# Kernel optimization log

Hardware: AMD Instinct MI355X
Metric: run time of the kernel (lower is better)

Reference implementation:

```python
import jax, jax.numpy as jnp
from jax import lax
import numpy as np

MB, N, QST, EPS = 512, 25, 11, 1e-5

def _coords():
    i = np.arange(25)
    # faithful to python3 true division: (i/5 - 2)/2.0, (i%5 - 2)/2.0
    c = np.stack([(i / 5 - 2) / 2.0, (i % 5 - 2) / 2.0], axis=-1).astype(np.float32)
    return jnp.asarray(c)  # [25, 2]

def _conv_bn(x, w, b, g, beta):
    # Conv2d(k=3, stride=2, pad=1) -> ReLU -> BatchNorm (training-mode batch stats)
    y = lax.conv_general_dilated(x, w, (2, 2), [(1, 1), (1, 1)],
                                 dimension_numbers=('NCHW', 'OIHW', 'NCHW'))
    y = jax.nn.relu(y + b[None, :, None, None])
    mean = y.mean(axis=(0, 2, 3), keepdims=True)
    var = y.var(axis=(0, 2, 3), keepdims=True)
    return (y - mean) * jax.lax.rsqrt(var + EPS) * g[None, :, None, None] + beta[None, :, None, None]

def setup_inputs() -> dict:
    key = jax.random.key(0)
    ks = jax.random.split(key, 20)
    w = lambda k, s: jax.random.normal(k, s, jnp.float32) * 0.05
    inp = {
        'img': jax.random.normal(ks[0], (MB, 3, 75, 75), jnp.float32),
        'qst': jax.random.normal(ks[1], (MB, QST), jnp.float32),
        'c1w': w(ks[2], (24, 3, 3, 3)),  'c1b': jnp.zeros((24,)), 'bn1g': jnp.ones((24,)), 'bn1b': jnp.zeros((24,)),
        'c2w': w(ks[3], (24, 24, 3, 3)), 'c2b': jnp.zeros((24,)), 'bn2g': jnp.ones((24,)), 'bn2b': jnp.zeros((24,)),
        'c3w': w(ks[4], (24, 24, 3, 3)), 'c3b': jnp.zeros((24,)), 'bn3g': jnp.ones((24,)), 'bn3b': jnp.zeros((24,)),
        'c4w': w(ks[5], (24, 24, 3, 3)), 'c4b': jnp.zeros((24,)), 'bn4g': jnp.ones((24,)), 'bn4b': jnp.zeros((24,)),
        'gw1': w(ks[6], (256, 63)),  'gb1': jnp.zeros((256,)),
        'gw2': w(ks[7], (256, 256)), 'gb2': jnp.zeros((256,)),
        'gw3': w(ks[8], (256, 256)), 'gb3': jnp.zeros((256,)),
        'gw4': w(ks[9], (256, 256)), 'gb4': jnp.zeros((256,)),
        'fw1': w(ks[10], (256, 256)), 'fb1': jnp.zeros((256,)),
        'fw2': w(ks[11], (256, 256)), 'fb2': jnp.zeros((256,)),
        'fw3': w(ks[12], (10, 256)),  'fb3': jnp.zeros((10,)),
    }
    return inp

def reference(img, qst, c1w, c1b, bn1g, bn1b, c2w, c2b, bn2g, bn2b,
              c3w, c3b, bn3g, bn3b, c4w, c4b, bn4g, bn4b,
              gw1, gb1, gw2, gb2, gw3, gb3, gw4, gb4,
              fw1, fb1, fw2, fb2, fw3, fb3):
    x = _conv_bn(img, c1w, c1b, bn1g, bn1b)
    x = _conv_bn(x, c2w, c2b, bn2g, bn2b)
    x = _conv_bn(x, c3w, c3b, bn3g, bn3b)
    x = _conv_bn(x, c4w, c4b, bn4g, bn4b)  # [mb, 24, 5, 5]
    mb, C = x.shape[0], x.shape[1]
    n = x.shape[2] * x.shape[3]
    xf = x.reshape(mb, C, n).transpose(0, 2, 1)              # [mb, N, 24]
    coord = jnp.broadcast_to(_coords()[None], (mb, n, 2))
    xf = jnp.concatenate([xf, coord], axis=-1)               # [mb, N, 26]
    qrep = jnp.broadcast_to(qst[:, None, :], (mb, n, QST))
    xj = jnp.concatenate([xf, qrep], axis=-1)                # [mb, N, 37]
    # pair[b,a,c] = [xf[b,c], xf[b,a], qst[b]]  (x_i varies over axis 2, x_j over axis 1)
    pair = jnp.concatenate([
        jnp.broadcast_to(xf[:, None, :, :], (mb, n, n, xf.shape[-1])),
        jnp.broadcast_to(xj[:, :, None, :], (mb, n, n, xj.shape[-1])),
    ], axis=-1)                                              # [mb, N, N, 63]
    h = pair.reshape(mb * n * n, -1)
    for w, b in ((gw1, gb1), (gw2, gb2), (gw3, gb3), (gw4, gb4)):
        h = jax.nn.relu(h @ w.T + b)
    xg = h.reshape(mb, n * n, 256).sum(axis=1)               # sum pooling over pairs
    y = jax.nn.relu(xg @ fw1.T + fb1)
    y = jax.nn.relu(y @ fw2.T + fb2)   # dropout treated as identity (eval mode)
    y = y @ fw3.T + fb3
    return jax.nn.log_softmax(y, axis=-1)
```

## Files before the change

kernel.cpp:

```cpp
#include <hip/hip_runtime.h>

typedef __bf16 bf16_t;
typedef __bf16 bf16x8 __attribute__((ext_vector_type(8)));
typedef __bf16 bf16x4 __attribute__((ext_vector_type(4)));
typedef float f32x16 __attribute__((ext_vector_type(16)));

#define MB 512
#define GROWS 128
#define GT_PER_B 5

__global__ __launch_bounds__(256, 4) void conv1_bn(const float* __restrict__ img,
                                                   const float* __restrict__ wT,
                                                   const float* __restrict__ bias,
                                                   float* __restrict__ out,
                                                   double* __restrict__ statsOut)
{
    __shared__ float in_s[3 * 39 * 77];
    __shared__ float red[48];
    int bid = blockIdx.x;
    int n = bid >> 1, tile = bid & 1;
    int oh0 = tile * 19;
    int tid = threadIdx.x;

    for (int idx = tid; idx < 3 * 39 * 77; idx += 256) {
        int ci = idx / (39 * 77);
        int rem = idx - ci * (39 * 77);
        int r = rem / 77, c = rem - r * 77;
        int ih = 2 * oh0 - 1 + r, iw = c - 1;
        float v = 0.f;
        if ((unsigned)ih < 75u && (unsigned)iw < 75u)
            v = img[((n * 3 + ci) * 75 + ih) * 75 + iw];
        in_s[idx] = v;
    }
    __syncthreads();

    int cg = tid >> 6, lane = tid & 63, co0 = cg * 6;
    int off[12];
    bool pv[12];
#pragma unroll
    for (int j = 0; j < 12; ++j) {
        int p = lane + j * 64;
        pv[j] = p < 722;
        int pc = pv[j] ? p : 0;
        int r0 = pc / 38, c0 = pc - r0 * 38;
        off[j] = (r0 * 2) * 77 + c0 * 2;
    }
    float acc[6][12];
#pragma unroll
    for (int c = 0; c < 6; ++c)
#pragma unroll
        for (int j = 0; j < 12; ++j) acc[c][j] = 0.f;

#pragma unroll 1
    for (int ci = 0; ci < 3; ++ci) {
        const float* ip = in_s + ci * (39 * 77);
        const float* wp = wT + ci * 9 * 24 + co0;
#pragma unroll
        for (int kh = 0; kh < 3; ++kh) {
#pragma unroll
            for (int kw = 0; kw < 3; ++kw) {
                float iv[12];
#pragma unroll
                for (int j = 0; j < 12; ++j) iv[j] = ip[off[j] + kh * 77 + kw];
                const float* wr = wp + (kh * 3 + kw) * 24;
                float2 w01 = *(const float2*)(wr);
                float2 w23 = *(const float2*)(wr + 2);
                float2 w45 = *(const float2*)(wr + 4);
#pragma unroll
                for (int j = 0; j < 12; ++j) {
                    acc[0][j] = fmaf(iv[j], w01.x, acc[0][j]);
                    acc[1][j] = fmaf(iv[j], w01.y, acc[1][j]);
                    acc[2][j] = fmaf(iv[j], w23.x, acc[2][j]);
                    acc[3][j] = fmaf(iv[j], w23.y, acc[3][j]);
                    acc[4][j] = fmaf(iv[j], w45.x, acc[4][j]);
                    acc[5][j] = fmaf(iv[j], w45.y, acc[5][j]);
                }
            }
        }
    }

    float sst[6], sq[6];
#pragma unroll
    for (int c = 0; c < 6; ++c) { sst[c] = 0.f; sq[c] = 0.f; }
#pragma unroll
    for (int c = 0; c < 6; ++c) {
        float bv = bias[co0 + c];
#pragma unroll
        for (int j = 0; j < 12; ++j) {
            if (pv[j]) {
                int p = lane + j * 64;
                int r = p / 38, q = p - r * 38;
                float v = fmaxf(acc[c][j] + bv, 0.f);
                out[((n * 24 + co0 + c) * 38 + oh0 + r) * 38 + q] = v;
                sst[c] += v; sq[c] += v * v;
            }
        }
    }
#pragma unroll
    for (int o = 1; o < 64; o <<= 1) {
#pragma unroll
        for (int c = 0; c < 6; ++c) {
            sst[c] += __shfl_xor(sst[c], o);
            sq[c]  += __shfl_xor(sq[c], o);
        }
    }
    if (lane == 0) {
#pragma unroll
        for (int c = 0; c < 6; ++c) {
            red[(co0 + c) * 2]     = sst[c];
            red[(co0 + c) * 2 + 1] = sq[c];
        }
    }
    __syncthreads();
    if (tid < 48) atomicAdd(&statsOut[tid], (double)red[tid]);
}

template <int HIN, int WIN, int HOUT, int WOUT, int OHT, int NP, int MINW>
__global__ __launch_bounds__(256, MINW) void conv24_bn(const float* __restrict__ in,
                                                    const float* __restrict__ wT,
                                                    const float* __restrict__ bias,
                                                    const double* __restrict__ statsIn,
                                                    const float* __restrict__ gIn,
                                                    const float* __restrict__ bIn, float invcntIn,
                                                    float* __restrict__ out,
                                                    double* __restrict__ statsOut, int tilesPerImg)
{
    constexpr int IR = 2 * OHT + 1;
    constexpr int ICW = 2 * WOUT + 1;
    __shared__ float in_s[24 * IR * ICW];
    __shared__ float aff[48];
    __shared__ float red[48];

    int bid = blockIdx.x;
    int n = bid / tilesPerImg, tile = bid - n * tilesPerImg;
    int oh0 = tile * OHT;
    int tid = threadIdx.x;

    if (tid < 24) {
        double meand = statsIn[tid * 2] * (double)invcntIn;
        double vard  = statsIn[tid * 2 + 1] * (double)invcntIn - meand * meand;
        float mean = (float)meand;
        float s    = gIn[tid] * rsqrtf((float)vard + 1e-5f);
        aff[tid * 2] = s;
        aff[tid * 2 + 1] = bIn[tid] - mean * s;
    }
    __syncthreads();
    for (int idx = tid; idx < 24 * IR * ICW; idx += 256) {
        int ci = idx / (IR * ICW);
        int rem = idx - ci * (IR * ICW);
        int r = rem / ICW, c = rem - r * ICW;
        int ih = 2 * oh0 - 1 + r, iw = c - 1;
        float v = 0.f;
        if ((unsigned)ih < (unsigned)HIN && (unsigned)iw < (unsigned)WIN)
            v = aff[ci * 2] * in[((n * 24 + ci) * HIN + ih) * WIN + iw] + aff[ci * 2 + 1];
        in_s[idx] = v;
    }
    __syncthreads();

    int cg = tid >> 6, lane = tid & 63, co0 = cg * 6;
    int nvr = HOUT - oh0; if (nvr > OHT) nvr = OHT;
    int nposv = nvr * WOUT;
    int off[NP];
    bool pv[NP];
#pragma unroll
    for (int j = 0; j < NP; ++j) {
        int p = lane + j * 64;
        pv[j] = p < nposv;
        int pc = pv[j] ? p : 0;
        int r0 = pc / WOUT, c0 = pc - r0 * WOUT;
        off[j] = (r0 * 2) * ICW + c0 * 2;
    }
    float acc[6][NP];
#pragma unroll
    for (int c = 0; c < 6; ++c)
#pragma unroll
        for (int j = 0; j < NP; ++j) acc[c][j] = 0.f;

#pragma unroll 1
    for (int ci = 0; ci < 24; ++ci) {
        const float* ip = in_s + ci * (IR * ICW);
        const float* wp = wT + ci * 9 * 24 + co0;
#pragma unroll
        for (int kh = 0; kh < 3; ++kh) {
#pragma unroll
            for (int kw = 0; kw < 3; ++kw) {
                float iv[NP];
#pragma unroll
                for (int j = 0; j < NP; ++j) iv[j] = ip[off[j] + kh * ICW + kw];
                const float* wr = wp + (kh * 3 + kw) * 24;
                float2 w01 = *(const float2*)(wr);
                float2 w23 = *(const float2*)(wr + 2);
                float2 w45 = *(const float2*)(wr + 4);
#pragma unroll
                for (int j = 0; j < NP; ++j) {
                    acc[0][j] = fmaf(iv[j], w01.x, acc[0][j]);
                    acc[1][j] = fmaf(iv[j], w01.y, acc[1][j]);
                    acc[2][j] = fmaf(iv[j], w23.x, acc[2][j]);
                    acc[3][j] = fmaf(iv[j], w23.y, acc[3][j]);
                    acc[4][j] = fmaf(iv[j], w45.x, acc[4][j]);
                    acc[5][j] = fmaf(iv[j], w45.y, acc[5][j]);
                }
            }
        }
    }

    float sst[6], sq[6];
#pragma unroll
    for (int c = 0; c < 6; ++c) { sst[c] = 0.f; sq[c] = 0.f; }
#pragma unroll
    for (int c = 0; c < 6; ++c) {
        float bv = bias[co0 + c];
#pragma unroll
        for (int j = 0; j < NP; ++j) {
            if (pv[j]) {
                int p = lane + j * 64;
                int r = p / WOUT, q = p - r * WOUT;
                float v = fmaxf(acc[c][j] + bv, 0.f);
                out[((n * 24 + co0 + c) * HOUT + oh0 + r) * WOUT + q] = v;
                sst[c] += v; sq[c] += v * v;
            }
        }
    }
#pragma unroll
    for (int o = 1; o < 64; o <<= 1) {
#pragma unroll
        for (int c = 0; c < 6; ++c) {
            sst[c] += __shfl_xor(sst[c], o);
            sq[c]  += __shfl_xor(sq[c], o);
        }
    }
    if (lane == 0) {
#pragma unroll
        for (int c = 0; c < 6; ++c) {
            red[(co0 + c) * 2]     = sst[c];
            red[(co0 + c) * 2 + 1] = sq[c];
        }
    }
    __syncthreads();
    if (tid < 48) atomicAdd(&statsOut[tid], (double)red[tid]);
}

__global__ void build_features(const float* __restrict__ y4, const double* __restrict__ stats4,
                               const float* __restrict__ g4, const float* __restrict__ b4,
                               const float* __restrict__ qst,
                               bf16_t* __restrict__ xf26, bf16_t* __restrict__ qstb)
{
    int idx = blockIdx.x * 256 + threadIdx.x;
    if (idx < MB * 11) qstb[idx] = (bf16_t)qst[idx];
    if (idx >= MB * 25) return;
    int b = idx / 25, p = idx % 25;
    const double invcnt = 1.0 / (MB * 25);
#pragma unroll
    for (int ch = 0; ch < 24; ++ch) {
        double meand = stats4[ch * 2] * invcnt;
        double vard  = stats4[ch * 2 + 1] * invcnt - meand * meand;
        float mean = (float)meand;
        float s    = g4[ch] * rsqrtf((float)vard + 1e-5f);
        float v    = s * y4[(b * 24 + ch) * 25 + p] + (b4[ch] - mean * s);
        xf26[idx * 26 + ch] = (bf16_t)v;
    }
    xf26[idx * 26 + 24] = (bf16_t)((p / 5.0f - 2.0f) * 0.5f);
    xf26[idx * 26 + 25] = (bf16_t)(((float)(p % 5) - 2.0f) * 0.5f);
}

__device__ __forceinline__ void frag256(int idx, const float* __restrict__ gw, bf16_t* __restrict__ Wf)
{
    int j = idx & 7, lane = (idx >> 3) & 63, ks = (idx >> 9) & 15, nt = idx >> 13;
    int n = nt * 32 + (lane & 31), k = ks * 16 + (lane >> 5) * 8 + j;
    Wf[idx] = (bf16_t)gw[n * 256 + k];
}

__global__ void prep_weights(const float* __restrict__ gw1, const float* __restrict__ gw2,
                             const float* __restrict__ gw3, const float* __restrict__ gw4,
                             const float* __restrict__ fw1, const float* __restrict__ fw2,
                             const float* __restrict__ c1w, const float* __restrict__ c2w,
                             const float* __restrict__ c3w, const float* __restrict__ c4w,
                             bf16_t* __restrict__ W1f, bf16_t* __restrict__ W2f,
                             bf16_t* __restrict__ W3f, bf16_t* __restrict__ W4f,
                             float* __restrict__ fw1T, float* __restrict__ fw2T,
                             float* __restrict__ wT1, float* __restrict__ wT2,
                             float* __restrict__ wT3, float* __restrict__ wT4)
{
    int idx = blockIdx.x * 256 + threadIdx.x;
    if (idx < 16384) {
        int j = idx & 7, lane = (idx >> 3) & 63, ks = (idx >> 9) & 3, nt = idx >> 11;
        int n = nt * 32 + (lane & 31), k = ks * 16 + (lane >> 5) * 8 + j;
        W1f[idx] = (k < 63) ? (bf16_t)gw1[n * 63 + k] : (bf16_t)0.0f;
        return;
    }
    idx -= 16384;
    if (idx < 65536) { frag256(idx, gw2, W2f); return; }
    idx -= 65536;
    if (idx < 65536) { frag256(idx, gw3, W3f); return; }
    idx -= 65536;
    if (idx < 65536) { frag256(idx, gw4, W4f); return; }
    idx -= 65536;
    if (idx < 65536) { int k = idx >> 8, nn = idx & 255; fw1T[idx] = fw1[nn * 256 + k]; return; }
    idx -= 65536;
    if (idx < 65536) { int k = idx >> 8, nn = idx & 255; fw2T[idx] = fw2[nn * 256 + k]; return; }
    idx -= 65536;
    if (idx < 648)   { int k = idx / 24, co = idx - k * 24; wT1[idx] = c1w[co * 27 + k]; return; }
    idx -= 648;
    if (idx < 5184)  { int k = idx / 24, co = idx - k * 24; wT2[idx] = c2w[co * 216 + k]; return; }
    idx -= 5184;
    if (idx < 5184)  { int k = idx / 24, co = idx - k * 24; wT3[idx] = c3w[co * 216 + k]; return; }
    idx -= 5184;
    if (idx < 5184)  { int k = idx / 24, co = idx - k * 24; wT4[idx] = c4w[co * 216 + k]; return; }
}


template <int NKS>
__device__ __forceinline__ void g_quarter(const bf16_t* hs, const bf16_t* __restrict__ wbase0,
                                          const bf16_t* __restrict__ wbase1,
                                          int q, int m31, int half,
                                          bf16x8 (&CUR)[2][4], bf16x8 (&NXT)[2][4],
                                          f32x16 (&acc)[4][2])
{
    if (q + 1 < NKS / 4) {
#pragma unroll
        for (int k = 0; k < 4; ++k) {
            NXT[0][k] = *(const bf16x8*)(wbase0 + (size_t)((q + 1) * 4 + k) * 512);
            NXT[1][k] = *(const bf16x8*)(wbase1 + (size_t)((q + 1) * 4 + k) * 512);
        }
    }
#pragma unroll
    for (int kk = 0; kk < 4; ++kk) {
        int ks = q * 4 + kk;
        int kc = ks * 2 + half;
        bf16x8 hf[4];
#pragma unroll
        for (int mt = 0; mt < 4; ++mt) {
            int m = mt * 32 + m31;
            hf[mt] = *(const bf16x8*)(hs + m * 256 + ((kc ^ m31) << 3));
        }
#pragma unroll
        for (int mt = 0; mt < 4; ++mt) {
            acc[mt][0] = __builtin_amdgcn_mfma_f32_32x32x16_bf16(CUR[0][kk], hf[mt], acc[mt][0], 0, 0, 0);
            acc[mt][1] = __builtin_amdgcn_mfma_f32_32x32x16_bf16(CUR[1][kk], hf[mt], acc[mt][1], 0, 0, 0);
        }
    }
}

template <int NKS>
__device__ __forceinline__ void g_layer(const bf16_t* hs, const bf16_t* __restrict__ Wf,
                                        int wid, int lane, f32x16 (&acc)[4][2])
{
    int m31 = lane & 31, half = lane >> 5;
#pragma unroll
    for (int mt = 0; mt < 4; ++mt)
#pragma unroll
        for (int nt = 0; nt < 2; ++nt) acc[mt][nt] = (f32x16)(0.f);

    const bf16_t* wbase0 = Wf + (size_t)(((wid * 2 + 0) * NKS) * 64 + lane) * 8;
    const bf16_t* wbase1 = Wf + (size_t)(((wid * 2 + 1) * NKS) * 64 + lane) * 8;
    bf16x8 wA[2][4], wB[2][4];
#pragma unroll
    for (int k = 0; k < 4; ++k) {
        wA[0][k] = *(const bf16x8*)(wbase0 + (size_t)k * 512);
        wA[1][k] = *(const bf16x8*)(wbase1 + (size_t)k * 512);
    }
#pragma unroll
    for (int q = 0; q < NKS / 4; ++q) {
        if ((q & 1) == 0) g_quarter<NKS>(hs, wbase0, wbase1, q, m31, half, wA, wB, acc);
        else              g_quarter<NKS>(hs, wbase0, wbase1, q, m31, half, wB, wA, acc);
    }
}

__device__ __forceinline__ void g_store(bf16_t* hs, const float* __restrict__ bias,
                                        int wid, int lane, f32x16 (&acc)[4][2])
{
    int m31 = lane & 31, half = lane >> 5;
#pragma unroll
    for (int mt = 0; mt < 4; ++mt) {
        int m = mt * 32 + m31;
#pragma unroll
        for (int nt = 0; nt < 2; ++nt) {
            int nbase = (wid * 2 + nt) * 32;
#pragma unroll
            for (int g = 0; g < 4; ++g) {
                int n0 = nbase + g * 8 + half * 4;
                float4 bv = *(const float4*)(bias + n0);
                bf16x4 v;
                v[0] = (bf16_t)fmaxf(acc[mt][nt][g * 4 + 0] + bv.x, 0.f);
                v[1] = (bf16_t)fmaxf(acc[mt][nt][g * 4 + 1] + bv.y, 0.f);
                v[2] = (bf16_t)fmaxf(acc[mt][nt][g * 4 + 2] + bv.z, 0.f);
                v[3] = (bf16_t)fmaxf(acc[mt][nt][g * 4 + 3] + bv.w, 0.f);
                int chunk = n0 >> 3;
                *(bf16x4*)(hs + m * 256 + ((chunk ^ m31) << 3) + (half << 2)) = v;
            }
        }
    }
}

__global__ void __launch_bounds__(256, 2)
g_mlp(const bf16_t* __restrict__ xf26, const bf16_t* __restrict__ qstb,
      const bf16_t* __restrict__ W1f, const bf16_t* __restrict__ W2f,
      const bf16_t* __restrict__ W3f, const bf16_t* __restrict__ W4f,
      const float* __restrict__ b1, const float* __restrict__ b2,
      const float* __restrict__ b3, const float* __restrict__ b4,
      float* __restrict__ xg5)
{
    __shared__ __align__(16) bf16_t hs[GROWS * 256];
    int b    = blockIdx.x / GT_PER_B;
    int tile = blockIdx.x % GT_PER_B;
    int tid  = threadIdx.x;

    for (int i = tid; i < GROWS * 8; i += 256) {
        int m = i >> 3, c = i & 7;
        int p = tile * GROWS + m;
        bf16x8 v;
        if (p < 625) {
            int a = p / 25, cp = p - a * 25;
            const bf16_t* f1 = xf26 + (b * 25 + cp) * 26;
            const bf16_t* f2 = xf26 + (b * 25 + a) * 26;
            const bf16_t* f3 = qstb + b * 11;
#pragma unroll
            for (int j = 0; j < 8; ++j) {
                int col = c * 8 + j;
                bf16_t u = (bf16_t)0.0f;
                if (col < 26) u = f1[col];
                else if (col < 52) u = f2[col - 26];
                else if (col < 63) u = f3[col - 52];
                v[j] = u;
            }
        } else {
#pragma unroll
            for (int j = 0; j < 8; ++j) v[j] = (bf16_t)0.0f;
        }
        *(bf16x8*)(hs + m * 256 + ((c ^ (m & 31)) << 3)) = v;
    }
    __syncthreads();

    int wid = tid >> 6, lane = tid & 63;
    int m31 = lane & 31, half = lane >> 5;
    f32x16 acc[4][2];

    g_layer<4>(hs, W1f, wid, lane, acc);
    __syncthreads(); g_store(hs, b1, wid, lane, acc); __syncthreads();
    g_layer<16>(hs, W2f, wid, lane, acc);
    __syncthreads(); g_store(hs, b2, wid, lane, acc); __syncthreads();
    g_layer<16>(hs, W3f, wid, lane, acc);
    __syncthreads(); g_store(hs, b3, wid, lane, acc); __syncthreads();
    g_layer<16>(hs, W4f, wid, lane, acc);

#pragma unroll
    for (int nt = 0; nt < 2; ++nt) {
        int nbase = (wid * 2 + nt) * 32;
        float bf[16];
#pragma unroll
        for (int r = 0; r < 16; ++r)
            bf[r] = b4[nbase + (r & 3) + 8 * (r >> 2) + 4 * half];
        f32x16 t = (f32x16)(0.f);
#pragma unroll
        for (int mt = 0; mt < 4; ++mt) {
            int p = tile * GROWS + mt * 32 + m31;
            if (p < 625) {
#pragma unroll
                for (int r = 0; r < 16; ++r)
                    t[r] += fmaxf(acc[mt][nt][r] + bf[r], 0.f);
            }
        }
#pragma unroll
        for (int off = 1; off < 32; off <<= 1) {
#pragma unroll
            for (int r = 0; r < 16; ++r) t[r] += __shfl_xor(t[r], off);
        }
        if (m31 == 0) {
#pragma unroll
            for (int r = 0; r < 16; ++r) {
                int nn = nbase + (r & 3) + 8 * (r >> 2) + 4 * half;
                xg5[(b * GT_PER_B + tile) * 256 + nn] = t[r];
            }
        }
    }
}

__global__ void f_mlp(const float* __restrict__ xg5, const float* __restrict__ fw1T, const float* __restrict__ fb1,
                      const float* __restrict__ fw2T, const float* __restrict__ fb2,
                      const float* __restrict__ fw3, const float* __restrict__ fb3,
                      float* __restrict__ out)
{
    __shared__ float xa[256], xb[256], lg[10];
    int b = blockIdx.x, t = threadIdx.x;
    float s0 = 0.f;
#pragma unroll
    for (int i = 0; i < GT_PER_B; ++i) s0 += xg5[(b * GT_PER_B + i) * 256 + t];
    xa[t] = s0;
    __syncthreads();
    float a = fb1[t];
    for (int k = 0; k < 256; ++k) a += fw1T[k * 256 + t] * xa[k];
    xb[t] = fmaxf(a, 0.f);
    __syncthreads();
    a = fb2[t];
    for (int k = 0; k < 256; ++k) a += fw2T[k * 256 + t] * xb[k];
    xa[t] = fmaxf(a, 0.f);
    __syncthreads();
    if (t < 10) {
        float s = fb3[t];
        for (int k = 0; k < 256; ++k) s += fw3[t * 256 + k] * xa[k];
        lg[t] = s;
    }
    __syncthreads();
    if (t == 0) {
        float m = lg[0];
        for (int i = 1; i < 10; ++i) m = fmaxf(m, lg[i]);
        float s = 0.f;
        for (int i = 0; i < 10; ++i) s += expf(lg[i] - m);
        float ls = m + logf(s);
        for (int i = 0; i < 10; ++i) out[b * 10 + i] = lg[i] - ls;
    }
}

extern "C" void kernel_launch(void* const* d_in, const int* in_sizes, int n_in,
                              void* d_out, int out_size, void* d_ws, size_t ws_size,
                              hipStream_t stream)
{
    (void)in_sizes; (void)n_in; (void)out_size; (void)ws_size;
    const float* img  = (const float*)d_in[0];
    const float* qst  = (const float*)d_in[1];
    const float* c1w  = (const float*)d_in[2];
    const float* c1b  = (const float*)d_in[3];
    const float* bn1g = (const float*)d_in[4];
    const float* bn1b = (const float*)d_in[5];
    const float* c2w  = (const float*)d_in[6];
    const float* c2b  = (const float*)d_in[7];
    const float* bn2g = (const float*)d_in[8];
    const float* bn2b = (const float*)d_in[9];
    const float* c3w  = (const float*)d_in[10];
    const float* c3b  = (const float*)d_in[11];
    const float* bn3g = (const float*)d_in[12];
    const float* bn3b = (const float*)d_in[13];
    const float* c4w  = (const float*)d_in[14];
    const float* c4b  = (const float*)d_in[15];
    const float* bn4g = (const float*)d_in[16];
    const float* bn4b = (const float*)d_in[17];
    const float* gw1  = (const float*)d_in[18];
    const float* gb1  = (const float*)d_in[19];
    const float* gw2  = (const float*)d_in[20];
    const float* gb2  = (const float*)d_in[21];
    const float* gw3  = (const float*)d_in[22];
    const float* gb3  = (const float*)d_in[23];
    const float* gw4  = (const float*)d_in[24];
    const float* gb4  = (const float*)d_in[25];
    const float* fw1  = (const float*)d_in[26];
    const float* fb1  = (const float*)d_in[27];
    const float* fw2  = (const float*)d_in[28];
    const float* fb2  = (const float*)d_in[29];
    const float* fw3  = (const float*)d_in[30];
    const float* fb3  = (const float*)d_in[31];

    const int Y1 = 512 * 24 * 38 * 38;
    const int Y2 = 512 * 24 * 19 * 19;
    const int Y3 = 512 * 24 * 10 * 10;
    const int Y4 = 512 * 24 * 5 * 5;

    double* stats = (double*)d_ws;
    float* fp = (float*)(stats + 192);
    float* y1    = fp;  fp += Y1;
    float* y2    = fp;  fp += Y2;
    float* y3    = fp;  fp += Y3;
    float* y4    = fp;  fp += Y4;
    float* xg5   = fp;  fp += 512 * GT_PER_B * 256;
    float* fw1T  = fp;  fp += 65536;
    float* fw2T  = fp;  fp += 65536;
    float* wT1   = fp;  fp += 648;
    float* wT2   = fp;  fp += 5184;
    float* wT3   = fp;  fp += 5184;
    float* wT4   = fp;  fp += 5184;
    bf16_t* bp   = (bf16_t*)fp;
    bf16_t* xf26 = bp;  bp += 512 * 25 * 26;
    bf16_t* qstb = bp;  bp += 512 * 11;
    bf16_t* W1f  = bp;  bp += 16384;
    bf16_t* W2f  = bp;  bp += 65536;
    bf16_t* W3f  = bp;  bp += 65536;
    bf16_t* W4f  = bp;  bp += 65536;

    hipMemsetAsync(stats, 0, 192 * sizeof(double), stream);

    prep_weights<<<1408, 256, 0, stream>>>(gw1, gw2, gw3, gw4, fw1, fw2, c1w, c2w, c3w, c4w,
                                           W1f, W2f, W3f, W4f, fw1T, fw2T,
                                           wT1, wT2, wT3, wT4);

    conv1_bn<<<1024, 256, 0, stream>>>(img, wT1, c1b, y1, stats + 0);

    conv24_bn<38, 38, 19, 19, 5, 2, 3><<<2048, 256, 0, stream>>>(
        y1, wT2, c2b, stats + 0, bn1g, bn1b, 1.f / (512.f * 1444.f),
        y2, stats + 48, 4);

    conv24_bn<19, 19, 10, 10, 10, 2, 3><<<512, 256, 0, stream>>>(
        y2, wT3, c3b, stats + 48, bn2g, bn2b, 1.f / (512.f * 361.f),
        y3, stats + 96, 1);

    conv24_bn<10, 10, 5, 5, 5, 1, 6><<<512, 256, 0, stream>>>(
        y3, wT4, c4b, stats + 96, bn3g, bn3b, 1.f / (512.f * 100.f),
        y4, stats + 144, 1);

    build_features<<<50, 256, 0, stream>>>(y4, stats + 144, bn4g, bn4b, qst, xf26, qstb);

    g_mlp<<<512 * GT_PER_B, 256, 0, stream>>>(xf26, qstb, W1f, W2f, W3f, W4f,
                                              gb1, gb2, gb3, gb4, xg5);

    f_mlp<<<512, 256, 0, stream>>>(xg5, fw1T, fb1, fw2T, fb2, fw3, fb3, (float*)d_out);
}
```

Baseline: 643.1 us.

## Shrink conv shared memory and tiles to raise occupancy

conv1 now splits each image into four row tiles of 10 output rows instead of two of 19, which halves its shared-memory footprint and per-thread accumulators, and launches twice as many blocks. The 24-channel conv kernels stage their input channels in two halves of 12 with an extra barrier, halving shared memory, and all use a launch bound of 6 waves. The aim is more resident blocks per CU to hide LDS and global latency. In exchange there are more halo loads and atomics in conv1, an extra sync phase in the conv24 kernels, and possible register pressure from the tighter launch bound.

```diff
diff --git a/kernel.cpp b/kernel.cpp
--- a/kernel.cpp
+++ b/kernel.cpp
@@ -9,22 +9,22 @@
 #define GROWS 128
 #define GT_PER_B 5
 
-__global__ __launch_bounds__(256, 4) void conv1_bn(const float* __restrict__ img,
+__global__ __launch_bounds__(256, 6) void conv1_bn(const float* __restrict__ img,
                                                    const float* __restrict__ wT,
                                                    const float* __restrict__ bias,
                                                    float* __restrict__ out,
                                                    double* __restrict__ statsOut)
 {
-    __shared__ float in_s[3 * 39 * 77];
+    __shared__ float in_s[3 * 21 * 77];
     __shared__ float red[48];
     int bid = blockIdx.x;
-    int n = bid >> 1, tile = bid & 1;
-    int oh0 = tile * 19;
+    int n = bid >> 2, tile = bid & 3;
+    int oh0 = tile * 10;
     int tid = threadIdx.x;
 
-    for (int idx = tid; idx < 3 * 39 * 77; idx += 256) {
-        int ci = idx / (39 * 77);
-        int rem = idx - ci * (39 * 77);
+    for (int idx = tid; idx < 3 * 21 * 77; idx += 256) {
+        int ci = idx / (21 * 77);
+        int rem = idx - ci * (21 * 77);
         int r = rem / 77, c = rem - r * 77;
         int ih = 2 * oh0 - 1 + r, iw = c - 1;
         float v = 0.f;
@@ -35,39 +35,41 @@
     __syncthreads();
 
     int cg = tid >> 6, lane = tid & 63, co0 = cg * 6;
-    int off[12];
-    bool pv[12];
-#pragma unroll
-    for (int j = 0; j < 12; ++j) {
+    int nvr = 38 - oh0; if (nvr > 10) nvr = 10;
+    int nposv = nvr * 38;
+    int off[6];
+    bool pv[6];
+#pragma unroll
+    for (int j = 0; j < 6; ++j) {
         int p = lane + j * 64;
-        pv[j] = p < 722;
+        pv[j] = p < nposv;
         int pc = pv[j] ? p : 0;
         int r0 = pc / 38, c0 = pc - r0 * 38;
         off[j] = (r0 * 2) * 77 + c0 * 2;
     }
-    float acc[6][12];
+    float acc[6][6];
 #pragma unroll
     for (int c = 0; c < 6; ++c)
 #pragma unroll
-        for (int j = 0; j < 12; ++j) acc[c][j] = 0.f;
+        for (int j = 0; j < 6; ++j) acc[c][j] = 0.f;
 
 #pragma unroll 1
     for (int ci = 0; ci < 3; ++ci) {
-        const float* ip = in_s + ci * (39 * 77);
+        const float* ip = in_s + ci * (21 * 77);
         const float* wp = wT + ci * 9 * 24 + co0;
 #pragma unroll
         for (int kh = 0; kh < 3; ++kh) {
 #pragma unroll
             for (int kw = 0; kw < 3; ++kw) {
-                float iv[12];
-#pragma unroll
-                for (int j = 0; j < 12; ++j) iv[j] = ip[off[j] + kh * 77 + kw];
+                float iv[6];
+#pragma unroll
+                for (int j = 0; j < 6; ++j) iv[j] = ip[off[j] + kh * 77 + kw];
                 const float* wr = wp + (kh * 3 + kw) * 24;
                 float2 w01 = *(const float2*)(wr);
                 float2 w23 = *(const float2*)(wr + 2);
                 float2 w45 = *(const float2*)(wr + 4);
 #pragma unroll
-                for (int j = 0; j < 12; ++j) {
+                for (int j = 0; j < 6; ++j) {
                     acc[0][j] = fmaf(iv[j], w01.x, acc[0][j]);
                     acc[1][j] = fmaf(iv[j], w01.y, acc[1][j]);
                     acc[2][j] = fmaf(iv[j], w23.x, acc[2][j]);
@@ -86,7 +88,7 @@
     for (int c = 0; c < 6; ++c) {
         float bv = bias[co0 + c];
 #pragma unroll
-        for (int j = 0; j < 12; ++j) {
+        for (int j = 0; j < 6; ++j) {
             if (pv[j]) {
                 int p = lane + j * 64;
                 int r = p / 38, q = p - r * 38;
@@ -115,8 +117,8 @@
     if (tid < 48) atomicAdd(&statsOut[tid], (double)red[tid]);
 }
 
-template <int HIN, int WIN, int HOUT, int WOUT, int OHT, int NP, int MINW>
-__global__ __launch_bounds__(256, MINW) void conv24_bn(const float* __restrict__ in,
+template <int HIN, int WIN, int HOUT, int WOUT, int OHT, int NP>
+__global__ __launch_bounds__(256, 6) void conv24_bn(const float* __restrict__ in,
                                                     const float* __restrict__ wT,
                                                     const float* __restrict__ bias,
                                                     const double* __restrict__ statsIn,
@@ -127,7 +129,8 @@
 {
     constexpr int IR = 2 * OHT + 1;
     constexpr int ICW = 2 * WOUT + 1;
-    __shared__ float in_s[24 * IR * ICW];
+    constexpr int CIB = 12;
+    __shared__ float in_s[CIB * IR * ICW];
     __shared__ float aff[48];
     __shared__ float red[48];
 
@@ -145,17 +148,6 @@
         aff[tid * 2 + 1] = bIn[tid] - mean * s;
     }
     __syncthreads();
-    for (int idx = tid; idx < 24 * IR * ICW; idx += 256) {
-        int ci = idx / (IR * ICW);
-        int rem = idx - ci * (IR * ICW);
-        int r = rem / ICW, c = rem - r * ICW;
-        int ih = 2 * oh0 - 1 + r, iw = c - 1;
-        float v = 0.f;
-        if ((unsigned)ih < (unsigned)HIN && (unsigned)iw < (unsigned)WIN)
-            v = aff[ci * 2] * in[((n * 24 + ci) * HIN + ih) * WIN + iw] + aff[ci * 2 + 1];
-        in_s[idx] = v;
-    }
-    __syncthreads();
 
     int cg = tid >> 6, lane = tid & 63, co0 = cg * 6;
     int nvr = HOUT - oh0; if (nvr > OHT) nvr = OHT;
@@ -177,28 +169,45 @@
         for (int j = 0; j < NP; ++j) acc[c][j] = 0.f;
 
 #pragma unroll 1
-    for (int ci = 0; ci < 24; ++ci) {
-        const float* ip = in_s + ci * (IR * ICW);
-        const float* wp = wT + ci * 9 * 24 + co0;
-#pragma unroll
-        for (int kh = 0; kh < 3; ++kh) {
-#pragma unroll
-            for (int kw = 0; kw < 3; ++kw) {
-                float iv[NP];
-#pragma unroll
-                for (int j = 0; j < NP; ++j) iv[j] = ip[off[j] + kh * ICW + kw];
-                const float* wr = wp + (kh * 3 + kw) * 24;
-                float2 w01 = *(const float2*)(wr);
-                float2 w23 = *(const float2*)(wr + 2);
-                float2 w45 = *(const float2*)(wr + 4);
-#pragma unroll
-                for (int j = 0; j < NP; ++j) {
-                    acc[0][j] = fmaf(iv[j], w01.x, acc[0][j]);
-                    acc[1][j] = fmaf(iv[j], w01.y, acc[1][j]);
-                    acc[2][j] = fmaf(iv[j], w23.x, acc[2][j]);
-                    acc[3][j] = fmaf(iv[j], w23.y, acc[3][j]);
-                    acc[4][j] = fmaf(iv[j], w45.x, acc[4][j]);
-                    acc[5][j] = fmaf(iv[j], w45.y, acc[5][j]);
+    for (int ph = 0; ph < 2; ++ph) {
+        if (ph) __syncthreads();
+        for (int idx = tid; idx < CIB * IR * ICW; idx += 256) {
+            int ci = idx / (IR * ICW);
+            int rem = idx - ci * (IR * ICW);
+            int r = rem / ICW, c = rem - r * ICW;
+            int gci = ph * CIB + ci;
+            int ih = 2 * oh0 - 1 + r, iw = c - 1;
+            float v = 0.f;
+            if ((unsigned)ih < (unsigned)HIN && (unsigned)iw < (unsigned)WIN)
+                v = aff[gci * 2] * in[((n * 24 + gci) * HIN + ih) * WIN + iw] + aff[gci * 2 + 1];
+            in_s[idx] = v;
+        }
+        __syncthreads();
+
+#pragma unroll 1
+        for (int ci = 0; ci < CIB; ++ci) {
+            const float* ip = in_s + ci * (IR * ICW);
+            const float* wp = wT + (ph * CIB + ci) * 9 * 24 + co0;
+#pragma unroll
+            for (int kh = 0; kh < 3; ++kh) {
+#pragma unroll
+                for (int kw = 0; kw < 3; ++kw) {
+                    float iv[NP];
+#pragma unroll
+                    for (int j = 0; j < NP; ++j) iv[j] = ip[off[j] + kh * ICW + kw];
+                    const float* wr = wp + (kh * 3 + kw) * 24;
+                    float2 w01 = *(const float2*)(wr);
+                    float2 w23 = *(const float2*)(wr + 2);
+                    float2 w45 = *(const float2*)(wr + 4);
+#pragma unroll
+                    for (int j = 0; j < NP; ++j) {
+                        acc[0][j] = fmaf(iv[j], w01.x, acc[0][j]);
+                        acc[1][j] = fmaf(iv[j], w01.y, acc[1][j]);
+                        acc[2][j] = fmaf(iv[j], w23.x, acc[2][j]);
+                        acc[3][j] = fmaf(iv[j], w23.y, acc[3][j]);
+                        acc[4][j] = fmaf(iv[j], w45.x, acc[4][j]);
+                        acc[5][j] = fmaf(iv[j], w45.y, acc[5][j]);
+                    }
                 }
             }
         }
@@ -581,17 +590,17 @@
                                            W1f, W2f, W3f, W4f, fw1T, fw2T,
                                            wT1, wT2, wT3, wT4);
 
-    conv1_bn<<<1024, 256, 0, stream>>>(img, wT1, c1b, y1, stats + 0);
-
-    conv24_bn<38, 38, 19, 19, 5, 2, 3><<<2048, 256, 0, stream>>>(
+    conv1_bn<<<2048, 256, 0, stream>>>(img, wT1, c1b, y1, stats + 0);
+
+    conv24_bn<38, 38, 19, 19, 5, 2><<<2048, 256, 0, stream>>>(
         y1, wT2, c2b, stats + 0, bn1g, bn1b, 1.f / (512.f * 1444.f),
         y2, stats + 48, 4);
 
-    conv24_bn<19, 19, 10, 10, 10, 2, 3><<<512, 256, 0, stream>>>(
+    conv24_bn<19, 19, 10, 10, 10, 2><<<512, 256, 0, stream>>>(
         y2, wT3, c3b, stats + 48, bn2g, bn2b, 1.f / (512.f * 361.f),
         y3, stats + 96, 1);
 
-    conv24_bn<10, 10, 5, 5, 5, 1, 6><<<512, 256, 0, stream>>>(
+    conv24_bn<10, 10, 5, 5, 5, 1><<<512, 256, 0, stream>>>(
         y3, wT4, c4b, stats + 96, bn3g, bn3b, 1.f / (512.f * 100.f),
         y4, stats + 144, 1);
 
```

New measurement: 606.7 us. 1.06x faster.
